# Optimization experiments

Hardware: AMD Instinct MI355X
Metric: run time of the kernel (lower is better)

Reference implementation:

```python
import jax, jax.numpy as jnp
import numpy as np

N_HEAD = 16
D_HEAD = 64
D_LATENT = 32
BLOCK_SIZE = 2048


def rope_cache(dim, max_seq_len, theta=10000.0):
    inv_freq = 1.0 / (theta ** (jnp.arange(0, dim, 2, dtype=jnp.float32) / dim))
    t = jnp.arange(max_seq_len, dtype=jnp.float32)
    freqs = jnp.einsum('i,j->ij', t, inv_freq)        # [T, dim/2]
    emb = jnp.concatenate([freqs, freqs], axis=-1)    # [T, dim]
    return jnp.cos(emb), jnp.sin(emb)


def apply_rope(x, cos, sin):
    # x: [B, H, T, C]; interleaved-pair rotation as in the torch module
    B, H, T, C = x.shape
    c = cos[:T][None, None]
    s = sin[:T][None, None]
    x1 = x[..., 0::2]
    x2 = x[..., 1::2]
    rotated = jnp.stack((-x2, x1), axis=-1).reshape(B, H, T, C)
    return x * c + rotated * s


def setup_inputs() -> dict:
    key = jax.random.key(0)
    ks = jax.random.split(key, 7)
    sd = 0.02
    return {
        'x':   jax.random.normal(ks[0], (2, 2048, 1024), dtype=jnp.float32),
        'Wq':  jax.random.normal(ks[1], (1024, 1024), dtype=jnp.float32) * sd,
        'Wk':  jax.random.normal(ks[2], (512, 1024), dtype=jnp.float32) * sd,
        'Wv':  jax.random.normal(ks[3], (512, 1024), dtype=jnp.float32) * sd,
        'Wku': jax.random.normal(ks[4], (64, 32), dtype=jnp.float32) * sd,
        'Wvu': jax.random.normal(ks[5], (64, 32), dtype=jnp.float32) * sd,
        'Wc':  jax.random.normal(ks[6], (1024, 1024), dtype=jnp.float32) * sd,
    }


def reference(x, Wq, Wk, Wv, Wku, Wvu, Wc):
    B, T, C = x.shape
    H, Dh, Dl = N_HEAD, D_HEAD, D_LATENT

    # latent KV (compressed cache entries)
    k_lat = (x @ Wk.T).reshape(B, T, H, Dl)   # [B,T,H,Dl]
    v_lat = (x @ Wv.T).reshape(B, T, H, Dl)

    # q and up-projected k/v -> [B,H,T,Dh]
    q = (x @ Wq.T).reshape(B, T, H, Dh).transpose(0, 2, 1, 3)
    k = jnp.einsum('bthl,dl->bhtd', k_lat, Wku)
    v = jnp.einsum('bthl,dl->bhtd', v_lat, Wvu)

    cos, sin = rope_cache(Dh, BLOCK_SIZE)
    q = apply_rope(q, cos, sin)
    k = apply_rope(k, cos, sin)

    scale = 1.0 / jnp.sqrt(jnp.asarray(Dh, dtype=x.dtype))
    att = jnp.einsum('bhqd,bhkd->bhqk', q, k) * scale   # [B,H,T,T]
    causal = jnp.tril(jnp.ones((T, T), dtype=bool))
    att = jnp.where(causal[None, None], att, -jnp.inf)
    att = jax.nn.softmax(att, axis=-1)

    y = jnp.einsum('bhqk,bhkd->bhqd', att, v)           # [B,H,T,Dh]
    y = y.transpose(0, 2, 1, 3).reshape(B, T, C) @ Wc.T  # [B,T,C]
    return y, k_lat, v_lat
```

## Files before the change

### kernel.cpp

```cpp
#include <hip/hip_runtime.h>
#include <math.h>

#define NHEAD  16
#define DHEAD  64
#define DLAT   32
#define TSEQ   2048
#define NBATCH 2
#define CDIM   1024
#define MROWS  (NBATCH*TSEQ)

typedef __attribute__((ext_vector_type(8))) short bf16x8;
typedef __attribute__((ext_vector_type(4))) short bf16x4;
typedef __attribute__((ext_vector_type(4))) float f32x4;

#define AS1 __attribute__((address_space(1)))
#define AS3 __attribute__((address_space(3)))

__device__ __forceinline__ unsigned short f2bf(float f) {
    union { float f; unsigned u; } v; v.f = f;
    unsigned r = v.u + 0x7fff + ((v.u >> 16) & 1);
    return (unsigned short)(r >> 16);
}

__device__ __forceinline__ unsigned pk2(float lo, float hi) {
    return (unsigned)f2bf(lo) | ((unsigned)f2bf(hi) << 16);
}

__device__ __forceinline__ unsigned pack_trunc(float hi, float lo) {
    return __builtin_amdgcn_perm(__float_as_uint(hi), __float_as_uint(lo), 0x07060302u);
}

__device__ __forceinline__ void gld_lds16(const unsigned short* g, unsigned short* l) {
    __builtin_amdgcn_global_load_lds((const AS1 void*)g, (AS3 void*)l, 16, 0, 0);
}

__device__ __forceinline__ f32x4 mfma_16x16x16_bf16(bf16x4 a, bf16x4 b, f32x4 c) {
#if __has_builtin(__builtin_amdgcn_mfma_f32_16x16x16bf16_1k)
    return __builtin_amdgcn_mfma_f32_16x16x16bf16_1k(a, b, c, 0, 0, 0);
#else
    asm volatile("v_mfma_f32_16x16x16_bf16 %0, %1, %2, %0\n\ts_nop 4"
                 : "+v"(c) : "v"(a), "v"(b));
    return c;
#endif
}

__global__ __launch_bounds__(256) void cvt_all(
        const float* __restrict__ x,  const float* __restrict__ wq,
        const float* __restrict__ wk, const float* __restrict__ wv,
        const float* __restrict__ wc, const float* __restrict__ wku,
        const float* __restrict__ wvu,
        unsigned short* __restrict__ xb, unsigned short* __restrict__ wall) {
    int i = (blockIdx.x * 256 + threadIdx.x) * 4;
    const float* src; unsigned short* dst; int off;
    if      (i < 4194304) { src = x;   dst = xb;             off = 0;       }
    else if (i < 5242880) { src = wq;  dst = wall;           off = 4194304; }
    else if (i < 5767168) { src = wk;  dst = wall + 1048576; off = 5242880; }
    else if (i < 6291456) { src = wv;  dst = wall + 1572864; off = 5767168; }
    else if (i < 7340032) { src = wc;  dst = wall + 2097152; off = 6291456; }
    else if (i < 7342080) { src = wku; dst = wall + 3145728; off = 7340032; }
    else                  { src = wvu; dst = wall + 3147776; off = 7342080; }
    float4 v = *(const float4*)(src + (i - off));
    ushort4 o = { f2bf(v.x), f2bf(v.y), f2bf(v.z), f2bf(v.w) };
    *(ushort4*)(dst + (i - off)) = o;
}

__device__ __forceinline__ void gemm_core(
        const unsigned short* __restrict__ A, const unsigned short* __restrict__ W,
        int K, int bm, int bn, unsigned short* As, unsigned short* Bs,
        f32x4 (&acc)[4][2]) {
    const int tid = threadIdx.x;
    const int w = tid >> 6, lane = tid & 63;
    const int quad = lane >> 4, l16 = lane & 15;
    const int wm = (w >> 2) * 64, wn = (w & 3) * 32;

    const int sr = tid >> 2;
    const int sc = (tid & 3) * 8;
    const unsigned short* Ag0 = A + (size_t)(bm + sr) * K + sc;
    const unsigned short* Wg0 = W + (size_t)(bn + sr) * K + sc;
    unsigned short* AsD = &As[(w*16) * 32];
    unsigned short* BsD = &Bs[(w*16) * 32];

    for (int k0 = 0; k0 < K; k0 += 32) {
        gld_lds16(Ag0 + k0, AsD);
        gld_lds16(Wg0 + k0, BsD);
        __syncthreads();
        bf16x8 af[4], bf[2];
        #pragma unroll
        for (int t = 0; t < 4; ++t)
            af[t] = *(const bf16x8*)&As[(wm + t*16 + l16)*32 + quad*8];
        #pragma unroll
        for (int c = 0; c < 2; ++c)
            bf[c] = *(const bf16x8*)&Bs[(wn + c*16 + l16)*32 + quad*8];
        #pragma unroll
        for (int t = 0; t < 4; ++t)
            #pragma unroll
            for (int c = 0; c < 2; ++c)
                acc[t][c] = __builtin_amdgcn_mfma_f32_16x16x32_bf16(af[t], bf[c], acc[t][c], 0, 0, 0);
        __syncthreads();
    }
}

__global__ __launch_bounds__(512) void gemm_proj(
        const unsigned short* __restrict__ A, const unsigned short* __restrict__ W,
        float* __restrict__ qproj, float* __restrict__ okl, float* __restrict__ ovl,
        int K) {
    __shared__ unsigned short As[128*32];
    __shared__ unsigned short Bs[128*32];
    const int bm = blockIdx.y * 128, bn = blockIdx.x * 128;
    f32x4 acc[4][2] = {};
    gemm_core(A, W, K, bm, bn, As, Bs, acc);

    const int tid = threadIdx.x;
    const int w = tid >> 6, lane = tid & 63;
    const int quad = lane >> 4, l16 = lane & 15;
    const int wm = (w >> 2) * 64, wn = (w & 3) * 32;

    float* base; int ldo;
    if (bn < 1024)      { base = qproj + bn;        ldo = 1024; }
    else if (bn < 1536) { base = okl + (bn - 1024); ldo = 512;  }
    else                { base = ovl + (bn - 1536); ldo = 512;  }

    #pragma unroll
    for (int t = 0; t < 4; ++t)
        #pragma unroll
        for (int c = 0; c < 2; ++c)
            #pragma unroll
            for (int r = 0; r < 4; ++r) {
                int row = bm + wm + t*16 + quad*4 + r;
                int col = wn + c*16 + l16;
                base[(size_t)row * ldo + col] = acc[t][c][r];
            }
}

__global__ __launch_bounds__(512) void gemm_out(
        const unsigned short* __restrict__ A, const unsigned short* __restrict__ W,
        float* __restrict__ O, int N, int K) {
    __shared__ unsigned short As[128*32];
    __shared__ unsigned short Bs[128*32];
    const int bm = blockIdx.y * 128, bn = blockIdx.x * 128;
    f32x4 acc[4][2] = {};
    gemm_core(A, W, K, bm, bn, As, Bs, acc);

    const int tid = threadIdx.x;
    const int w = tid >> 6, lane = tid & 63;
    const int quad = lane >> 4, l16 = lane & 15;
    const int wm = (w >> 2) * 64, wn = (w & 3) * 32;
    #pragma unroll
    for (int t = 0; t < 4; ++t)
        #pragma unroll
        for (int c = 0; c < 2; ++c)
            #pragma unroll
            for (int r = 0; r < 4; ++r) {
                int row = bm + wm + t*16 + quad*4 + r;
                int col = bn + wn + c*16 + l16;
                O[(size_t)row * N + col] = acc[t][c][r];
            }
}

#define QSCALE 0.18033688011112042f
__global__ __launch_bounds__(256) void latup(
        const float* __restrict__ qproj, const float* __restrict__ klat,
        const float* __restrict__ vlat,
        const unsigned short* __restrict__ wkub, const unsigned short* __restrict__ wvub,
        unsigned short* __restrict__ qb, unsigned short* __restrict__ kb,
        unsigned short* __restrict__ vt) {
    __shared__ __attribute__((aligned(16))) unsigned short ksh[4][16][72];
    __shared__ __attribute__((aligned(16))) unsigned short qsh[4][16][72];
    __shared__ __attribute__((aligned(16))) unsigned short vsh[4][64][24];

    const int bh = blockIdx.y, b = bh >> 4, h = bh & 15;
    const int tid = threadIdx.x, w = tid >> 6, lane = tid & 63;
    const int quad = lane >> 4, l16 = lane & 15;
    const int tw = blockIdx.x * 64 + w * 16;
    const int t  = tw + l16;

    const float* klp = klat + ((size_t)(b*TSEQ + t))*(NHEAD*DLAT) + h*DLAT + quad*8;
    const float* vlp = vlat + ((size_t)(b*TSEQ + t))*(NHEAD*DLAT) + h*DLAT + quad*8;
    float4 kA = *(const float4*)klp, kB = *(const float4*)(klp + 4);
    float4 vA = *(const float4*)vlp, vB = *(const float4*)(vlp + 4);

    bf16x8 xk[4], xv[4];
    #pragma unroll
    for (int c = 0; c < 4; ++c) {
        xk[c] = *(const bf16x8*)&wkub[(c*16 + l16)*DLAT + quad*8];
        xv[c] = *(const bf16x8*)&wvub[(c*16 + l16)*DLAT + quad*8];
    }

    union { bf16x8 v; unsigned u[4]; } yk, yv;
    yk.u[0] = pk2(kA.x, kA.y); yk.u[1] = pk2(kA.z, kA.w);
    yk.u[2] = pk2(kB.x, kB.y); yk.u[3] = pk2(kB.z, kB.w);
    yv.u[0] = pk2(vA.x, vA.y); yv.u[1] = pk2(vA.z, vA.w);
    yv.u[2] = pk2(vB.x, vB.y); yv.u[3] = pk2(vB.z, vB.w);

    f32x4 aK[4], aV[4];
    #pragma unroll
    for (int c = 0; c < 4; ++c) {
        f32x4 z = {0.f, 0.f, 0.f, 0.f};
        aK[c] = __builtin_amdgcn_mfma_f32_16x16x32_bf16(xk[c], yk.v, z, 0, 0, 0);
        aV[c] = __builtin_amdgcn_mfma_f32_16x16x32_bf16(xv[c], yv.v, z, 0, 0, 0);
    }

    float C0[4], S0[4], C1[4], S1[4];
    const float tf = (float)t;
    #pragma unroll
    for (int j = 0; j < 4; ++j) {
        float f0 = (float)(quad*4 + j);
        __sincosf(tf * __expf(-f0 * 0.28782313662425572f),          &S0[j], &C0[j]);
        __sincosf(tf * __expf(-(f0 + 16.f) * 0.28782313662425572f), &S1[j], &C1[j]);
    }

    const float* qrow = qproj + ((size_t)(b*TSEQ + t))*CDIM + h*DHEAD;
    #pragma unroll
    for (int c = 0; c < 4; ++c) {
        const float* Cs = (c & 1) ? C1 : C0;
        const float* Ss = (c & 1) ? S1 : S0;
        float a0 = aK[c][0], a1 = aK[c][1], a2 = aK[c][2], a3 = aK[c][3];
        unsigned kw0 = pk2(a0*Cs[0] - a1*Ss[0], a1*Cs[1] + a0*Ss[1]);
        unsigned kw1 = pk2(a2*Cs[2] - a3*Ss[2], a3*Cs[3] + a2*Ss[3]);
        *(uint2*)&ksh[w][l16][c*16 + quad*4] = make_uint2(kw0, kw1);

        float4 qv = *(const float4*)(qrow + c*16 + quad*4);
        unsigned qw0 = pk2((qv.x*Cs[0] - qv.y*Ss[0])*QSCALE, (qv.y*Cs[1] + qv.x*Ss[1])*QSCALE);
        unsigned qw1 = pk2((qv.z*Cs[2] - qv.w*Ss[2])*QSCALE, (qv.w*Cs[3] + qv.z*Ss[3])*QSCALE);
        *(uint2*)&qsh[w][l16][c*16 + quad*4] = make_uint2(qw0, qw1);

        vsh[w][c*16 + quad*4 + 0][l16] = f2bf(aV[c][0]);
        vsh[w][c*16 + quad*4 + 1][l16] = f2bf(aV[c][1]);
        vsh[w][c*16 + quad*4 + 2][l16] = f2bf(aV[c][2]);
        vsh[w][c*16 + quad*4 + 3][l16] = f2bf(aV[c][3]);
    }

    __asm__ __volatile__("s_waitcnt lgkmcnt(0)" ::: "memory");

    const int ro = lane >> 2, co = (lane & 3) * 16;
    size_t go = ((size_t)bh*TSEQ + tw + ro)*DHEAD + co;
    int4 k0o = *(const int4*)&ksh[w][ro][co];
    int4 k1o = *(const int4*)&ksh[w][ro][co + 8];
    *(int4*)&kb[go]     = k0o;
    *(int4*)&kb[go + 8] = k1o;
    int4 q0o = *(const int4*)&qsh[w][ro][co];
    int4 q1o = *(const int4*)&qsh[w][ro][co + 8];
    *(int4*)&qb[go]     = q0o;
    *(int4*)&qb[go + 8] = q1o;

    size_t vo = ((size_t)bh*DHEAD + lane)*TSEQ + tw;
    int4 v0o = *(const int4*)&vsh[w][lane][0];
    int4 v1o = *(const int4*)&vsh[w][lane][8];
    *(int4*)&vt[vo]     = v0o;
    *(int4*)&vt[vo + 8] = v1o;
}

__global__ __launch_bounds__(256, 4) void flash_attn(
        const unsigned short* __restrict__ qb, const unsigned short* __restrict__ kb,
        const unsigned short* __restrict__ vtb, unsigned short* __restrict__ yatt) {
    const int bh = blockIdx.x;
    const int qt = 31 - (int)blockIdx.y;
    const int b = bh >> 4, h = bh & 15;

    __shared__ unsigned short Ks[2][64][64];
    __shared__ unsigned short VTs[2][64][64];

    const int tid  = threadIdx.x;
    const int wq   = tid >> 6;
    const int lane = tid & 63;
    const int quad = lane >> 4;
    const int l16  = lane & 15;

    const unsigned short* Kbase = kb  + (size_t)bh * TSEQ * DHEAD;
    const unsigned short* Vbase = vtb + (size_t)bh * DHEAD * TSEQ;

    const int r8  = lane >> 3;
    const int c8  = lane & 7;
    const int scl = (c8 ^ r8) * 8;

    const int kx0 = (quad ^ (l16 & 7)) * 8;
    const int kx1 = ((quad + 4) ^ (l16 & 7)) * 8;
    const int vq = (quad >> 1), vodd = (quad & 1) * 4;

    const int n64 = qt + 1;

    const unsigned short* qbase =
        qb + ((size_t)bh*TSEQ + qt*64 + wq*16 + l16) * DHEAD + quad*8;
    bf16x8 q0 = *(const bf16x8*)qbase;
    bf16x8 q1 = *(const bf16x8*)(qbase + 32);

    f32x4 oacc[4] = {};
    float m_run = -1e30f, l_run = 0.f;

    #pragma unroll
    for (int i = 0; i < 2; ++i) {
        gld_lds16(Kbase + (size_t)(wq*16 + i*8 + r8)*DHEAD + scl,
                  &Ks[0][wq*16 + i*8][0]);
        gld_lds16(Vbase + (size_t)(wq*16 + i*8 + r8)*TSEQ + scl,
                  &VTs[0][wq*16 + i*8][0]);
    }
    __syncthreads();

    for (int j = 0; j < n64; ++j) {
        const int buf = j & 1;
        if (j + 1 < n64) {
            const int kc = (j + 1) * 64;
            #pragma unroll
            for (int i = 0; i < 2; ++i) {
                gld_lds16(Kbase + (size_t)(kc + wq*16 + i*8 + r8)*DHEAD + scl,
                          &Ks[buf^1][wq*16 + i*8][0]);
                gld_lds16(Vbase + (size_t)(wq*16 + i*8 + r8)*TSEQ + kc + scl,
                          &VTs[buf^1][wq*16 + i*8][0]);
            }
        }

        f32x4 s[4];
        __builtin_amdgcn_s_setprio(1);
        #pragma unroll
        for (int c = 0; c < 4; ++c) {
            bf16x8 ak0 = *(const bf16x8*)&Ks[buf][c*16 + l16][kx0];
            bf16x8 ak1 = *(const bf16x8*)&Ks[buf][c*16 + l16][kx1];
            f32x4 z = {0.f, 0.f, 0.f, 0.f};
            z = __builtin_amdgcn_mfma_f32_16x16x32_bf16(ak0, q0, z, 0, 0, 0);
            z = __builtin_amdgcn_mfma_f32_16x16x32_bf16(ak1, q1, z, 0, 0, 0);
            s[c] = z;
        }
        __builtin_amdgcn_s_setprio(0);

        if (j == n64 - 1) {
            #pragma unroll
            for (int c = 0; c < 4; ++c)
                #pragma unroll
                for (int r = 0; r < 4; ++r)
                    if (c*16 + quad*4 + r > wq*16 + l16)
                        s[c][r] = -1e30f;
        }

        float mx = -1e30f;
        #pragma unroll
        for (int c = 0; c < 4; ++c)
            #pragma unroll
            for (int r = 0; r < 4; ++r) mx = fmaxf(mx, s[c][r]);
        mx = fmaxf(mx, __shfl_xor(mx, 16, 64));
        mx = fmaxf(mx, __shfl_xor(mx, 32, 64));
        if (!__all(mx <= m_run + 8.f)) {
            float mn = fmaxf(m_run, mx);
            float alpha = __builtin_exp2f(m_run - mn);
            m_run = mn;
            l_run *= alpha;
            #pragma unroll
            for (int c = 0; c < 4; ++c)
                #pragma unroll
                for (int r = 0; r < 4; ++r) oacc[c][r] *= alpha;
        }
        float ls = 0.f;
        #pragma unroll
        for (int c = 0; c < 4; ++c)
            #pragma unroll
            for (int r = 0; r < 4; ++r) {
                float p = __builtin_exp2f(s[c][r] - m_run);
                s[c][r] = p;
                ls += p;
            }
        ls += __shfl_xor(ls, 16, 64);
        ls += __shfl_xor(ls, 32, 64);
        l_run += ls;

        __builtin_amdgcn_s_setprio(1);
        #pragma unroll
        for (int c = 0; c < 4; ++c) {
            union { bf16x4 v; unsigned u[2]; } bP;
            bP.u[0] = pack_trunc(s[c][1], s[c][0]);
            bP.u[1] = pack_trunc(s[c][3], s[c][2]);
            const int vcol = ((2*c + vq) ^ (l16 & 7)) * 8 + vodd;
            #pragma unroll
            for (int dc = 0; dc < 4; ++dc) {
                bf16x4 av = *(const bf16x4*)&VTs[buf][dc*16 + l16][vcol];
                oacc[dc] = mfma_16x16x16_bf16(av, bP.v, oacc[dc]);
            }
        }
        __builtin_amdgcn_s_setprio(0);

        __syncthreads();
    }

    float invl = 1.0f / l_run;
    unsigned short* Wt = &Ks[0][0][0] + wq * (16*72);
    #pragma unroll
    for (int c = 0; c < 4; ++c)
        #pragma unroll
        for (int r = 0; r < 4; ++r)
            Wt[(size_t)l16*72 + c*16 + quad*4 + r] = f2bf(oacc[c][r] * invl);
    __asm__ __volatile__("" ::: "memory");
    #pragma unroll
    for (int p = 0; p < 2; ++p) {
        int row = p*8 + (lane >> 3);
        int d0 = (lane & 7) * 8;
        int4 val = *(const int4*)&Wt[row*72 + d0];
        int tg = qt*64 + wq*16 + row;
        *(int4*)&yatt[((size_t)(b*TSEQ + tg))*CDIM + h*DHEAD + d0] = val;
    }
}

extern "C" void kernel_launch(void* const* d_in, const int* in_sizes, int n_in,
                              void* d_out, int out_size, void* d_ws, size_t ws_size,
                              hipStream_t stream) {
    const float* x   = (const float*)d_in[0];
    const float* Wq  = (const float*)d_in[1];
    const float* Wk  = (const float*)d_in[2];
    const float* Wv  = (const float*)d_in[3];
    const float* Wku = (const float*)d_in[4];
    const float* Wvu = (const float*)d_in[5];
    const float* Wc  = (const float*)d_in[6];

    float* out_y  = (float*)d_out;
    float* out_kl = out_y  + (size_t)MROWS * CDIM;
    float* out_vl = out_kl + (size_t)MROWS * NHEAD*DLAT;

    float* qproj = (float*)d_ws;
    unsigned short* xb   = (unsigned short*)(qproj + (size_t)MROWS*CDIM);
    unsigned short* qb   = xb  + (size_t)MROWS*CDIM;
    unsigned short* kb   = qb  + (size_t)MROWS*CDIM;
    unsigned short* vt   = kb  + (size_t)MROWS*CDIM;
    unsigned short* wall = vt  + (size_t)MROWS*CDIM;
    unsigned short* wcb  = wall + (size_t)2048*CDIM;
    unsigned short* wkub = wall + 3145728;
    unsigned short* wvub = wall + 3147776;
    unsigned short* yatt = (unsigned short*)qproj;

    cvt_all<<<7172, 256, 0, stream>>>(x, Wq, Wk, Wv, Wc, Wku, Wvu, xb, wall);

    gemm_proj<<<dim3(2048/128, MROWS/128), 512, 0, stream>>>(
        xb, wall, qproj, out_kl, out_vl, CDIM);

    latup<<<dim3(TSEQ/64, NBATCH*NHEAD), 256, 0, stream>>>(
        qproj, out_kl, out_vl, wkub, wvub, qb, kb, vt);

    flash_attn<<<dim3(NBATCH*NHEAD, 32), 256, 0, stream>>>(qb, kb, vt, yatt);

    gemm_out<<<dim3(CDIM/128, MROWS/128), 512, 0, stream>>>(yatt, wcb, out_y, CDIM, CDIM);
}
```

Before: 200.3 us.

## Pair light and heavy query tiles per attention block and shrink GEMM tiles

Flash attention now runs 512-thread blocks in which four waves handle a short causal query tile and four handle the matching long one, sharing 128-key K/V tiles loaded into LDS. The aim is to balance causal work per block and halve the number of K/V tile iterations. The GEMMs move to 128x64 output tiles with more blocks and an occupancy hint of four blocks, which gives more parallelism at the cost of less reuse per block. The light waves sit idle at barriers once their tile is finished.

```diff
diff --git a/kernel.cpp b/kernel.cpp
--- a/kernel.cpp
+++ b/kernel.cpp
@@ -67,11 +67,11 @@
 __device__ __forceinline__ void gemm_core(
         const unsigned short* __restrict__ A, const unsigned short* __restrict__ W,
         int K, int bm, int bn, unsigned short* As, unsigned short* Bs,
-        f32x4 (&acc)[4][2]) {
+        f32x4 (&acc)[2][2]) {
     const int tid = threadIdx.x;
     const int w = tid >> 6, lane = tid & 63;
     const int quad = lane >> 4, l16 = lane & 15;
-    const int wm = (w >> 2) * 64, wn = (w & 3) * 32;
+    const int wm = (w >> 1) * 32, wn = (w & 1) * 32;
 
     const int sr = tid >> 2;
     const int sc = (tid & 3) * 8;
@@ -82,17 +82,17 @@
 
     for (int k0 = 0; k0 < K; k0 += 32) {
         gld_lds16(Ag0 + k0, AsD);
-        gld_lds16(Wg0 + k0, BsD);
+        if (w < 4) gld_lds16(Wg0 + k0, BsD);
         __syncthreads();
-        bf16x8 af[4], bf[2];
-        #pragma unroll
-        for (int t = 0; t < 4; ++t)
+        bf16x8 af[2], bf[2];
+        #pragma unroll
+        for (int t = 0; t < 2; ++t)
             af[t] = *(const bf16x8*)&As[(wm + t*16 + l16)*32 + quad*8];
         #pragma unroll
         for (int c = 0; c < 2; ++c)
             bf[c] = *(const bf16x8*)&Bs[(wn + c*16 + l16)*32 + quad*8];
         #pragma unroll
-        for (int t = 0; t < 4; ++t)
+        for (int t = 0; t < 2; ++t)
             #pragma unroll
             for (int c = 0; c < 2; ++c)
                 acc[t][c] = __builtin_amdgcn_mfma_f32_16x16x32_bf16(af[t], bf[c], acc[t][c], 0, 0, 0);
@@ -100,20 +100,20 @@
     }
 }
 
-__global__ __launch_bounds__(512) void gemm_proj(
+__global__ __launch_bounds__(512, 4) void gemm_proj(
         const unsigned short* __restrict__ A, const unsigned short* __restrict__ W,
         float* __restrict__ qproj, float* __restrict__ okl, float* __restrict__ ovl,
         int K) {
     __shared__ unsigned short As[128*32];
-    __shared__ unsigned short Bs[128*32];
-    const int bm = blockIdx.y * 128, bn = blockIdx.x * 128;
-    f32x4 acc[4][2] = {};
+    __shared__ unsigned short Bs[64*32];
+    const int bm = blockIdx.y * 128, bn = blockIdx.x * 64;
+    f32x4 acc[2][2] = {};
     gemm_core(A, W, K, bm, bn, As, Bs, acc);
 
     const int tid = threadIdx.x;
     const int w = tid >> 6, lane = tid & 63;
     const int quad = lane >> 4, l16 = lane & 15;
-    const int wm = (w >> 2) * 64, wn = (w & 3) * 32;
+    const int wm = (w >> 1) * 32, wn = (w & 1) * 32;
 
     float* base; int ldo;
     if (bn < 1024)      { base = qproj + bn;        ldo = 1024; }
@@ -121,7 +121,7 @@
     else                { base = ovl + (bn - 1536); ldo = 512;  }
 
     #pragma unroll
-    for (int t = 0; t < 4; ++t)
+    for (int t = 0; t < 2; ++t)
         #pragma unroll
         for (int c = 0; c < 2; ++c)
             #pragma unroll
@@ -132,21 +132,21 @@
             }
 }
 
-__global__ __launch_bounds__(512) void gemm_out(
+__global__ __launch_bounds__(512, 4) void gemm_out(
         const unsigned short* __restrict__ A, const unsigned short* __restrict__ W,
         float* __restrict__ O, int N, int K) {
     __shared__ unsigned short As[128*32];
-    __shared__ unsigned short Bs[128*32];
-    const int bm = blockIdx.y * 128, bn = blockIdx.x * 128;
-    f32x4 acc[4][2] = {};
+    __shared__ unsigned short Bs[64*32];
+    const int bm = blockIdx.y * 128, bn = blockIdx.x * 64;
+    f32x4 acc[2][2] = {};
     gemm_core(A, W, K, bm, bn, As, Bs, acc);
 
     const int tid = threadIdx.x;
     const int w = tid >> 6, lane = tid & 63;
     const int quad = lane >> 4, l16 = lane & 15;
-    const int wm = (w >> 2) * 64, wn = (w & 3) * 32;
-    #pragma unroll
-    for (int t = 0; t < 4; ++t)
+    const int wm = (w >> 1) * 32, wn = (w & 1) * 32;
+    #pragma unroll
+    for (int t = 0; t < 2; ++t)
         #pragma unroll
         for (int c = 0; c < 2; ++c)
             #pragma unroll
@@ -250,34 +250,72 @@
     *(int4*)&vt[vo + 8] = v1o;
 }
 
-__global__ __launch_bounds__(256, 4) void flash_attn(
+__device__ __forceinline__ void online_sm(f32x4 (&s)[8], float& m_run, float& l_run,
+                                          f32x4 (&o)[4]) {
+    float mx = -1e30f;
+    #pragma unroll
+    for (int c = 0; c < 8; ++c)
+        #pragma unroll
+        for (int r = 0; r < 4; ++r) mx = fmaxf(mx, s[c][r]);
+    mx = fmaxf(mx, __shfl_xor(mx, 16, 64));
+    mx = fmaxf(mx, __shfl_xor(mx, 32, 64));
+    if (!__all(mx <= m_run + 8.f)) {
+        float mn = fmaxf(m_run, mx);
+        float alpha = __builtin_exp2f(m_run - mn);
+        m_run = mn;
+        l_run *= alpha;
+        #pragma unroll
+        for (int c = 0; c < 4; ++c)
+            #pragma unroll
+            for (int r = 0; r < 4; ++r) o[c][r] *= alpha;
+    }
+    float ls = 0.f;
+    #pragma unroll
+    for (int c = 0; c < 8; ++c)
+        #pragma unroll
+        for (int r = 0; r < 4; ++r) {
+            float p = __builtin_exp2f(s[c][r] - m_run);
+            s[c][r] = p;
+            ls += p;
+        }
+    ls += __shfl_xor(ls, 16, 64);
+    ls += __shfl_xor(ls, 32, 64);
+    l_run += ls;
+}
+
+__global__ __launch_bounds__(512, 4) void flash_attn(
         const unsigned short* __restrict__ qb, const unsigned short* __restrict__ kb,
         const unsigned short* __restrict__ vtb, unsigned short* __restrict__ yatt) {
     const int bh = blockIdx.x;
-    const int qt = 31 - (int)blockIdx.y;
     const int b = bh >> 4, h = bh & 15;
 
-    __shared__ unsigned short Ks[2][64][64];
-    __shared__ unsigned short VTs[2][64][64];
+    __shared__ unsigned short Ks[2][128][64];
+    __shared__ unsigned short VTs[2][64][128];
 
     const int tid  = threadIdx.x;
-    const int wq   = tid >> 6;
+    const int w    = tid >> 6;
     const int lane = tid & 63;
     const int quad = lane >> 4;
     const int l16  = lane & 15;
+    const bool heavy = (w >= 4);
+    const int wq = w & 3;
+
+    const int qtA = blockIdx.y;
+    const int qtB = 31 - qtA;
+    const int qt  = heavy ? qtB : qtA;
+    const int myN = (qt + 2) >> 1;
+    const int nB  = (qtB + 2) >> 1;
 
     const unsigned short* Kbase = kb  + (size_t)bh * TSEQ * DHEAD;
     const unsigned short* Vbase = vtb + (size_t)bh * DHEAD * TSEQ;
 
-    const int r8  = lane >> 3;
-    const int c8  = lane & 7;
-    const int scl = (c8 ^ r8) * 8;
+    const int kr8 = lane >> 3, kc8 = lane & 7;
+    const int kcl = (kc8 ^ kr8) * 8;
+    const int vr4 = lane >> 4, vcp = lane & 15;
 
     const int kx0 = (quad ^ (l16 & 7)) * 8;
     const int kx1 = ((quad + 4) ^ (l16 & 7)) * 8;
     const int vq = (quad >> 1), vodd = (quad & 1) * 4;
-
-    const int n64 = qt + 1;
 
     const unsigned short* qbase =
         qb + ((size_t)bh*TSEQ + qt*64 + wq*16 + l16) * DHEAD + quad*8;
@@ -289,98 +327,75 @@
 
     #pragma unroll
     for (int i = 0; i < 2; ++i) {
-        gld_lds16(Kbase + (size_t)(wq*16 + i*8 + r8)*DHEAD + scl,
-                  &Ks[0][wq*16 + i*8][0]);
-        gld_lds16(Vbase + (size_t)(wq*16 + i*8 + r8)*TSEQ + scl,
-                  &VTs[0][wq*16 + i*8][0]);
+        gld_lds16(Kbase + (size_t)(w*16 + i*8 + kr8)*DHEAD + kcl,
+                  &Ks[0][w*16 + i*8][0]);
+        int vrow = w*8 + i*4 + vr4;
+        int vcl = (vcp ^ (vrow & 15)) * 8;
+        gld_lds16(Vbase + (size_t)vrow*TSEQ + vcl, &VTs[0][w*8 + i*4][0]);
     }
     __syncthreads();
 
-    for (int j = 0; j < n64; ++j) {
+    for (int j = 0; j < nB; ++j) {
         const int buf = j & 1;
-        if (j + 1 < n64) {
-            const int kc = (j + 1) * 64;
+        if (j + 1 < nB) {
+            const int kc = (j + 1) * 128;
             #pragma unroll
             for (int i = 0; i < 2; ++i) {
-                gld_lds16(Kbase + (size_t)(kc + wq*16 + i*8 + r8)*DHEAD + scl,
-                          &Ks[buf^1][wq*16 + i*8][0]);
-                gld_lds16(Vbase + (size_t)(wq*16 + i*8 + r8)*TSEQ + kc + scl,
-                          &VTs[buf^1][wq*16 + i*8][0]);
+                gld_lds16(Kbase + (size_t)(kc + w*16 + i*8 + kr8)*DHEAD + kcl,
+                          &Ks[buf^1][w*16 + i*8][0]);
+                int vrow = w*8 + i*4 + vr4;
+                int vcl = (vcp ^ (vrow & 15)) * 8;
+                gld_lds16(Vbase + (size_t)vrow*TSEQ + kc + vcl,
+                          &VTs[buf^1][w*8 + i*4][0]);
             }
         }
 
-        f32x4 s[4];
-        __builtin_amdgcn_s_setprio(1);
-        #pragma unroll
-        for (int c = 0; c < 4; ++c) {
-            bf16x8 ak0 = *(const bf16x8*)&Ks[buf][c*16 + l16][kx0];
-            bf16x8 ak1 = *(const bf16x8*)&Ks[buf][c*16 + l16][kx1];
-            f32x4 z = {0.f, 0.f, 0.f, 0.f};
-            z = __builtin_amdgcn_mfma_f32_16x16x32_bf16(ak0, q0, z, 0, 0, 0);
-            z = __builtin_amdgcn_mfma_f32_16x16x32_bf16(ak1, q1, z, 0, 0, 0);
-            s[c] = z;
+        if (j < myN) {
+            f32x4 s[8];
+            __builtin_amdgcn_s_setprio(1);
+            #pragma unroll
+            for (int c = 0; c < 8; ++c) {
+                bf16x8 ak0 = *(const bf16x8*)&Ks[buf][c*16 + l16][kx0];
+                bf16x8 ak1 = *(const bf16x8*)&Ks[buf][c*16 + l16][kx1];
+                f32x4 z = {0.f, 0.f, 0.f, 0.f};
+                z = __builtin_amdgcn_mfma_f32_16x16x32_bf16(ak0, q0, z, 0, 0, 0);
+                z = __builtin_amdgcn_mfma_f32_16x16x32_bf16(ak1, q1, z, 0, 0, 0);
+                s[c] = z;
+            }
+            __builtin_amdgcn_s_setprio(0);
+
+            if (j == myN - 1) {
+                #pragma unroll
+                for (int c = 0; c < 8; ++c)
+                    #pragma unroll
+                    for (int r = 0; r < 4; ++r)
+                        if (j*128 + c*16 + quad*4 + r > qt*64 + wq*16 + l16)
+                            s[c][r] = -1e30f;
+            }
+
+            online_sm(s, m_run, l_run, oacc);
+
+            __builtin_amdgcn_s_setprio(1);
+            #pragma unroll
+            for (int c = 0; c < 8; ++c) {
+                union { bf16x4 v; unsigned u[2]; } bP;
+                bP.u[0] = pack_trunc(s[c][1], s[c][0]);
+                bP.u[1] = pack_trunc(s[c][3], s[c][2]);
+                const int vcol = ((2*c + vq) ^ l16) * 8 + vodd;
+                #pragma unroll
+                for (int dc = 0; dc < 4; ++dc) {
+                    bf16x4 av = *(const bf16x4*)&VTs[buf][dc*16 + l16][vcol];
+                    oacc[dc] = mfma_16x16x16_bf16(av, bP.v, oacc[dc]);
+                }
+            }
+            __builtin_amdgcn_s_setprio(0);
         }
-        __builtin_amdgcn_s_setprio(0);
-
-        if (j == n64 - 1) {
-            #pragma unroll
-            for (int c = 0; c < 4; ++c)
-                #pragma unroll
-                for (int r = 0; r < 4; ++r)
-                    if (c*16 + quad*4 + r > wq*16 + l16)
-                        s[c][r] = -1e30f;
-        }
-
-        float mx = -1e30f;
-        #pragma unroll
-        for (int c = 0; c < 4; ++c)
-            #pragma unroll
-            for (int r = 0; r < 4; ++r) mx = fmaxf(mx, s[c][r]);
-        mx = fmaxf(mx, __shfl_xor(mx, 16, 64));
-        mx = fmaxf(mx, __shfl_xor(mx, 32, 64));
-        if (!__all(mx <= m_run + 8.f)) {
-            float mn = fmaxf(m_run, mx);
-            float alpha = __builtin_exp2f(m_run - mn);
-            m_run = mn;
-            l_run *= alpha;
-            #pragma unroll
-            for (int c = 0; c < 4; ++c)
-                #pragma unroll
-                for (int r = 0; r < 4; ++r) oacc[c][r] *= alpha;
-        }
-        float ls = 0.f;
-        #pragma unroll
-        for (int c = 0; c < 4; ++c)
-            #pragma unroll
-            for (int r = 0; r < 4; ++r) {
-                float p = __builtin_exp2f(s[c][r] - m_run);
-                s[c][r] = p;
-                ls += p;
-            }
-        ls += __shfl_xor(ls, 16, 64);
-        ls += __shfl_xor(ls, 32, 64);
-        l_run += ls;
-
-        __builtin_amdgcn_s_setprio(1);
-        #pragma unroll
-        for (int c = 0; c < 4; ++c) {
-            union { bf16x4 v; unsigned u[2]; } bP;
-            bP.u[0] = pack_trunc(s[c][1], s[c][0]);
-            bP.u[1] = pack_trunc(s[c][3], s[c][2]);
-            const int vcol = ((2*c + vq) ^ (l16 & 7)) * 8 + vodd;
-            #pragma unroll
-            for (int dc = 0; dc < 4; ++dc) {
-                bf16x4 av = *(const bf16x4*)&VTs[buf][dc*16 + l16][vcol];
-                oacc[dc] = mfma_16x16x16_bf16(av, bP.v, oacc[dc]);
-            }
-        }
-        __builtin_amdgcn_s_setprio(0);
 
         __syncthreads();
     }
 
     float invl = 1.0f / l_run;
-    unsigned short* Wt = &Ks[0][0][0] + wq * (16*72);
+    unsigned short* Wt = &Ks[0][0][0] + w * (16*72);
     #pragma unroll
     for (int c = 0; c < 4; ++c)
         #pragma unroll
@@ -425,13 +440,13 @@
 
     cvt_all<<<7172, 256, 0, stream>>>(x, Wq, Wk, Wv, Wc, Wku, Wvu, xb, wall);
 
-    gemm_proj<<<dim3(2048/128, MROWS/128), 512, 0, stream>>>(
+    gemm_proj<<<dim3(2048/64, MROWS/128), 512, 0, stream>>>(
         xb, wall, qproj, out_kl, out_vl, CDIM);
 
     latup<<<dim3(TSEQ/64, NBATCH*NHEAD), 256, 0, stream>>>(
         qproj, out_kl, out_vl, wkub, wvub, qb, kb, vt);
 
-    flash_attn<<<dim3(NBATCH*NHEAD, 32), 256, 0, stream>>>(qb, kb, vt, yatt);
-
-    gemm_out<<<dim3(CDIM/128, MROWS/128), 512, 0, stream>>>(yatt, wcb, out_y, CDIM, CDIM);
-}
+    flash_attn<<<dim3(NBATCH*NHEAD, 16), 512, 0, stream>>>(qb, kb, vt, yatt);
+
+    gemm_out<<<dim3(CDIM/64, MROWS/128), 512, 0, stream>>>(yatt, wcb, out_y, CDIM, CDIM);
+}
```

Measured after the change: 191.6 us. 4.3% less time.
